# Performance work log

Measured on AMD Instinct MI355X. Metric: run time of the kernel, lower is better.

Reference implementation:

```python
import jax, jax.numpy as jnp
import numpy as np

DIM = 512
HEADS = 8
DIM_HEAD = 64
INNER = HEADS * DIM_HEAD  # 512
LN_EPS = 1e-5


def setup_inputs() -> dict:
    key = jax.random.key(0)
    ks = jax.random.split(key, 6)
    b, n = 2, 2048
    x = jax.random.normal(ks[0], (b, n, DIM), dtype=jnp.float32)
    # to_qkv: Linear(dim, inner*3, bias=False); torch weight is [out,in], apply as x @ W.T
    w_qkv = jax.random.normal(ks[1], (3 * INNER, DIM), dtype=jnp.float32) * (DIM ** -0.5)
    reattn_w = jax.random.normal(ks[2], (HEADS, HEADS), dtype=jnp.float32)
    ln_g = jnp.ones((HEADS,), dtype=jnp.float32)
    ln_b = jnp.zeros((HEADS,), dtype=jnp.float32)
    w_out = jax.random.normal(ks[3], (DIM, INNER), dtype=jnp.float32) * (INNER ** -0.5)
    b_out = jnp.zeros((DIM,), dtype=jnp.float32)
    return {"x": x, "w_qkv": w_qkv, "reattn_w": reattn_w,
            "ln_g": ln_g, "ln_b": ln_b, "w_out": w_out, "b_out": b_out}


def reference(x, w_qkv, reattn_w, ln_g, ln_b, w_out, b_out):
    b, n, _ = x.shape
    scale = DIM_HEAD ** -0.5
    qkv = x @ w_qkv.T  # [b, n, 3*inner]
    q, k, v = jnp.split(qkv, 3, axis=-1)
    # b n (h d) -> b h n d
    split_heads = lambda t: t.reshape(b, n, HEADS, DIM_HEAD).transpose(0, 2, 1, 3)
    q, k, v = split_heads(q), split_heads(k), split_heads(v)
    dots = jnp.einsum('bhid,bhjd->bhij', q, k) * scale
    attn = jax.nn.softmax(dots, axis=-1)
    # re-attention: cross-head mixing then LayerNorm over head dim
    attn = jnp.einsum('bhij,hg->bgij', attn, reattn_w)
    a = attn.transpose(0, 2, 3, 1)  # b i j h
    mu = jnp.mean(a, axis=-1, keepdims=True)
    var = jnp.mean((a - mu) ** 2, axis=-1, keepdims=True)
    a = (a - mu) * jax.lax.rsqrt(var + LN_EPS) * ln_g + ln_b
    attn = a.transpose(0, 3, 1, 2)  # b h i j
    out = jnp.einsum('bhij,bhjd->bhid', attn, v)
    out = out.transpose(0, 2, 1, 3).reshape(b, n, INNER)
    out = out @ w_out.T + b_out  # dropout p=0 -> identity
    return out
```

## Files before the change

### kernel.cpp

```cpp
#include <hip/hip_runtime.h>
#include <hip/hip_bf16.h>


typedef __attribute__((ext_vector_type(8))) short bfx8;
typedef __attribute__((ext_vector_type(4))) float f32x4;
typedef unsigned short u16;
typedef unsigned int u32;

#define QSCALE 0.18033688011112042f

static __device__ inline u16 f2bf(float f) {
  union { float f; unsigned u; } cv; cv.f = f;
  unsigned u = cv.u;
  u += 0x7fffu + ((u >> 16) & 1u);
  return (u16)(u >> 16);
}
static __device__ inline u32 cvtpk(float lo, float hi) {
  u32 d; asm("v_cvt_pk_bf16_f32 %0, %1, %2" : "=v"(d) : "v"(lo), "v"(hi)); return d;
}
static __device__ inline float fexp2(float x) {
  float r; asm("v_exp_f32 %0, %1" : "=v"(r) : "v"(x)); return r;
}
static __device__ inline float flog2(float x) {
  float r; asm("v_log_f32 %0, %1" : "=v"(r) : "v"(x)); return r;
}

__global__ __launch_bounds__(256) void convert3(
    const float* __restrict__ x, const float* __restrict__ wq,
    const float* __restrict__ wo,
    u16* __restrict__ xb, u16* __restrict__ wqb, u16* __restrict__ wob) {
  int e = (blockIdx.x * 256 + threadIdx.x) * 4;
  const float* src; u16* dst; int off;
  if (e < 2097152)      { src = x;  dst = xb;  off = e; }
  else if (e < 2883584) { src = wq; dst = wqb; off = e - 2097152; }
  else                  { src = wo; dst = wob; off = e - 2883584; }
  float4 v = *(const float4*)&src[off];
  ushort4 o; o.x = f2bf(v.x); o.y = f2bf(v.y); o.z = f2bf(v.z); o.w = f2bf(v.w);
  *(ushort4*)&dst[off] = o;
}

__global__ __launch_bounds__(256) void gemm_qkv(
    const u16* __restrict__ A, const u16* __restrict__ B,
    u16* __restrict__ qb, u16* __restrict__ kb, u16* __restrict__ vtb) {
  __shared__ u16 As[128 * 32];
  __shared__ u16 Bs[128 * 32];
  const int t = threadIdx.x, lane = t & 63;
  const int wm = (t >> 6) >> 1, wn = (t >> 6) & 1;
  const int m0 = blockIdx.y * 128, n0 = blockIdx.x * 128;
  const int li = lane & 15, lg = lane >> 4;
  const int rowA = t >> 2, kb8 = (t & 3) * 8;
  f32x4 acc[4][4] = {};
  for (int k0 = 0; k0 < 512; k0 += 32) {
    __syncthreads();
    *(bfx8*)&As[rowA * 32 + kb8]        = *(const bfx8*)&A[(size_t)(m0 + rowA) * 512 + k0 + kb8];
    *(bfx8*)&As[(rowA + 64) * 32 + kb8] = *(const bfx8*)&A[(size_t)(m0 + rowA + 64) * 512 + k0 + kb8];
    *(bfx8*)&Bs[rowA * 32 + kb8]        = *(const bfx8*)&B[(size_t)(n0 + rowA) * 512 + k0 + kb8];
    *(bfx8*)&Bs[(rowA + 64) * 32 + kb8] = *(const bfx8*)&B[(size_t)(n0 + rowA + 64) * 512 + k0 + kb8];
    __syncthreads();
    bfx8 af[4], bf_[4];
#pragma unroll
    for (int mi = 0; mi < 4; mi++)
      af[mi] = *(const bfx8*)&As[(wm * 64 + mi * 16 + li) * 32 + lg * 8];
#pragma unroll
    for (int ni = 0; ni < 4; ni++)
      bf_[ni] = *(const bfx8*)&Bs[(wn * 64 + ni * 16 + li) * 32 + lg * 8];
#pragma unroll
    for (int mi = 0; mi < 4; mi++)
#pragma unroll
      for (int ni = 0; ni < 4; ni++)
        acc[mi][ni] = __builtin_amdgcn_mfma_f32_16x16x32_bf16(af[mi], bf_[ni], acc[mi][ni], 0, 0, 0);
  }
#pragma unroll
  for (int mi = 0; mi < 4; mi++) {
#pragma unroll
    for (int ni = 0; ni < 4; ni++) {
      const int nc  = n0 + wn * 64 + ni * 16 + li;
      const int mrb = m0 + wm * 64 + mi * 16 + lg * 4;
      const int part = nc >> 9, within = nc & 511;
      const int h = within >> 6, d = within & 63;
      const int bb = mrb >> 11, ii = mrb & 2047;
      if (part == 0) {
#pragma unroll
        for (int r = 0; r < 4; r++)
          qb[(((size_t)bb * 8 + h) * 2048 + ii + r) * 64 + d] = f2bf(acc[mi][ni][r] * QSCALE);
      } else if (part == 1) {
#pragma unroll
        for (int r = 0; r < 4; r++)
          kb[(((size_t)bb * 8 + h) * 2048 + ii + r) * 64 + d] = f2bf(acc[mi][ni][r]);
      } else {
        ushort4 u;
        u.x = f2bf(acc[mi][ni][0]); u.y = f2bf(acc[mi][ni][1]);
        u.z = f2bf(acc[mi][ni][2]); u.w = f2bf(acc[mi][ni][3]);
        *(ushort4*)&vtb[(((size_t)bb * 8 + h) * 64 + d) * 2048 + ii] = u;
      }
    }
  }
}

__global__ __launch_bounds__(256) void passA(
    const u16* __restrict__ qb, const u16* __restrict__ kb,
    float2* __restrict__ statp) {
  const int t = threadIdx.x, lane = t & 63, w = t >> 6;
  const int bh = blockIdx.y, js = blockIdx.z;
  const int i0 = blockIdx.x * 64 + w * 16;
  const int li = lane & 15, lg = lane >> 4;
  const u16* Qh = qb + ((size_t)bh * 2048 + i0 + li) * 64;
  const u16* Kb = kb + (size_t)bh * 2048 * 64;
  const bfx8 q0 = *(const bfx8*)&Qh[lg * 8];
  const bfx8 q1 = *(const bfx8*)&Qh[32 + lg * 8];
  float m = -1e30f, l = 0.f;
  const int jbeg = js * 512, jend = jbeg + 512;
  for (int j0 = jbeg; j0 < jend; j0 += 32) {
    const u16* KhA = Kb + (size_t)(j0 + li) * 64;
    const u16* KhB = KhA + 16 * 64;
    bfx8 a0 = *(const bfx8*)&KhA[lg * 8];
    bfx8 a1 = *(const bfx8*)&KhA[32 + lg * 8];
    bfx8 b0 = *(const bfx8*)&KhB[lg * 8];
    bfx8 b1 = *(const bfx8*)&KhB[32 + lg * 8];
    __builtin_amdgcn_sched_barrier(0);
    f32x4 sa = {0.f, 0.f, 0.f, 0.f}, sb = {0.f, 0.f, 0.f, 0.f};
    sa = __builtin_amdgcn_mfma_f32_16x16x32_bf16(a0, q0, sa, 0, 0, 0);
    sa = __builtin_amdgcn_mfma_f32_16x16x32_bf16(a1, q1, sa, 0, 0, 0);
    sb = __builtin_amdgcn_mfma_f32_16x16x32_bf16(b0, q0, sb, 0, 0, 0);
    sb = __builtin_amdgcn_mfma_f32_16x16x32_bf16(b1, q1, sb, 0, 0, 0);
    float mt = fmaxf(fmaxf(fmaxf(sa[0], sa[1]), fmaxf(sa[2], sa[3])),
                     fmaxf(fmaxf(sb[0], sb[1]), fmaxf(sb[2], sb[3])));
    float mn = fmaxf(m, mt);
    float es = (fexp2(sa[0] - mn) + fexp2(sa[1] - mn)) + (fexp2(sa[2] - mn) + fexp2(sa[3] - mn))
             + (fexp2(sb[0] - mn) + fexp2(sb[1] - mn)) + (fexp2(sb[2] - mn) + fexp2(sb[3] - mn));
    l = fmaf(l, fexp2(m - mn), es);
    m = mn;
  }
  for (int off = 16; off < 64; off <<= 1) {
    float mo = __shfl_xor(m, off, 64);
    float lo = __shfl_xor(l, off, 64);
    float mn = fmaxf(m, mo);
    l = l * fexp2(m - mn) + lo * fexp2(mo - mn);
    m = mn;
  }
  if (lane < 16) statp[(size_t)js * 32768 + (size_t)bh * 2048 + i0 + li] = make_float2(m, l);
}

__global__ __launch_bounds__(512) __attribute__((amdgpu_waves_per_eu(4, 4)))
void passB(
    const u16* __restrict__ qb, const u16* __restrict__ kb,
    const u16* __restrict__ vtb, const float2* __restrict__ statp,
    const float* __restrict__ Wmix, const float* __restrict__ lng,
    const float* __restrict__ lnb, u16* __restrict__ innerP) {
  __shared__ __align__(16) u16 A2[8 * 16 * 128];
  __shared__ __align__(16) u16 Qs[8 * 16 * 72];
  const int t = threadIdx.x, lane = t & 63, w = t >> 6;
  const int b = blockIdx.y, i0 = blockIdx.x * 16;
  const int li = lane & 15, lg = lane >> 4;
  const int swz = (li & 7) << 3;

#pragma unroll
  for (int cc = 0; cc < 2; cc++) {
    const int c = t + cc * 512;
    const int h = c >> 7, qi = (c >> 3) & 15, d8 = c & 7;
    bfx8 v = *(const bfx8*)&qb[(((size_t)(b * 8 + h)) * 2048 + i0 + qi) * 64 + d8 * 8];
    *(bfx8*)&Qs[(h * 16 + qi) * 72 + d8 * 8] = v;
  }

  float wm_[8][8], lng_[8], lnb_[8];
#pragma unroll
  for (int h = 0; h < 8; h++)
#pragma unroll
    for (int g = 0; g < 8; g++) wm_[h][g] = Wmix[h * 8 + g];
#pragma unroll
  for (int g = 0; g < 8; g++) { lng_[g] = lng[g]; lnb_[g] = lnb[g]; }

  float stM[8];
#pragma unroll
  for (int h = 0; h < 8; h++) {
    const size_t idx = ((size_t)(b * 8 + h)) * 2048 + i0 + li;
    float m = -1e30f, l = 0.f;
#pragma unroll
    for (int z = 0; z < 4; z++) {
      const float2 a = statp[(size_t)z * 32768 + idx];
      const float mn = fmaxf(m, a.x);
      l = l * fexp2(m - mn) + a.y * fexp2(a.x - mn);
      m = mn;
    }
    stM[h] = m + flog2(l);
  }

  __syncthreads();

  f32x4 pacc[4] = {};
  const int jmb = blockIdx.z * 1024;
  const size_t hstr = (size_t)2048 * 64;
  for (int jm = jmb; jm < jmb + 1024; jm += 128) {
    const int j0 = jm + w * 16;
    const u16* Kb0 = kb + ((size_t)(b * 8) * 2048 + j0 + li) * 64;
    float p[8][4];
#pragma unroll
    for (int hb = 0; hb < 2; hb++) {
      bfx8 kf[4][2];
#pragma unroll
      for (int hh = 0; hh < 4; hh++) {
        const u16* Kh = Kb0 + (size_t)(hb * 4 + hh) * hstr;
        kf[hh][0] = *(const bfx8*)&Kh[lg * 8];
        kf[hh][1] = *(const bfx8*)&Kh[32 + lg * 8];
      }
      __builtin_amdgcn_sched_barrier(0);
#pragma unroll
      for (int hh = 0; hh < 4; hh++) {
        const int h = hb * 4 + hh;
        const bfx8 qA = *(const bfx8*)&Qs[(h * 16 + li) * 72 + lg * 8];
        const bfx8 qB = *(const bfx8*)&Qs[(h * 16 + li) * 72 + 32 + lg * 8];
        f32x4 s = {0.f, 0.f, 0.f, 0.f};
        s = __builtin_amdgcn_mfma_f32_16x16x32_bf16(kf[hh][0], qA, s, 0, 0, 0);
        s = __builtin_amdgcn_mfma_f32_16x16x32_bf16(kf[hh][1], qB, s, 0, 0, 0);
#pragma unroll
        for (int r = 0; r < 4; r++) p[h][r] = fexp2(s[r] - stM[h]);
      }
    }
    u32 apk[8][2];
#pragma unroll
    for (int r = 0; r < 4; r++) {
      float a_[8]; float sum = 0.f, sumsq = 0.f;
#pragma unroll
      for (int g = 0; g < 8; g++) {
        float acc = 0.f;
#pragma unroll
        for (int h = 0; h < 8; h++) acc = fmaf(p[h][r], wm_[h][g], acc);
        a_[g] = acc; sum += acc; sumsq = fmaf(acc, acc, sumsq);
      }
      const float mu = sum * 0.125f;
      const float var = fmaf(sumsq, 0.125f, -mu * mu);
      const float rs = rsqrtf(var + 1e-5f);
#pragma unroll
      for (int g = 0; g < 8; g++) {
        const float av = fmaf((a_[g] - mu) * rs, lng_[g], lnb_[g]);
        if (r & 1) apk[g][r >> 1] |= cvtpk(av, av) & 0xffff0000u;
        else       apk[g][r >> 1]  = cvtpk(av, av) & 0x0000ffffu;
      }
    }
    {
      const int jsw = (w * 16 + lg * 4) ^ swz;
#pragma unroll
      for (int g = 0; g < 8; g++)
        *(uint2*)&A2[(g * 16 + li) * 128 + jsw] = make_uint2(apk[g][0], apk[g][1]);
    }
    const u16* Vh = vtb + ((size_t)(b * 8 + w)) * 64 * 2048 + jm;
    bfx8 vF[4][4];
#pragma unroll
    for (int kc = 0; kc < 4; kc++)
#pragma unroll
      for (int nd = 0; nd < 4; nd++)
        vF[kc][nd] = *(const bfx8*)&Vh[(size_t)(nd * 16 + li) * 2048 + kc * 32 + lg * 8];
    __syncthreads();
    __builtin_amdgcn_s_setprio(1);
#pragma unroll
    for (int kc = 0; kc < 4; kc++) {
      const bfx8 af = *(const bfx8*)&A2[(w * 16 + li) * 128 + ((kc * 32 + lg * 8) ^ swz)];
#pragma unroll
      for (int nd = 0; nd < 4; nd++)
        pacc[nd] = __builtin_amdgcn_mfma_f32_16x16x32_bf16(af, vF[kc][nd], pacc[nd], 0, 0, 0);
    }
    __builtin_amdgcn_s_setprio(0);
    __syncthreads();
  }
  u16* dst = innerP + (size_t)blockIdx.z * 2097152 + ((size_t)b * 2048 + i0) * 512 + w * 64;
#pragma unroll
  for (int nd = 0; nd < 4; nd++)
#pragma unroll
    for (int r = 0; r < 4; r++)
      dst[(lg * 4 + r) * 512 + nd * 16 + li] = f2bf(pacc[nd][r]);
}

static __device__ inline bfx8 addbf8(bfx8 a, bfx8 b) {
  bfx8 r;
#pragma unroll
  for (int e = 0; e < 8; e += 2) {
    union { float f; u32 u; } a0, a1, b0, b1;
    a0.u = ((u32)(u16)a[e]) << 16;     b0.u = ((u32)(u16)b[e]) << 16;
    a1.u = ((u32)(u16)a[e + 1]) << 16; b1.u = ((u32)(u16)b[e + 1]) << 16;
    const u32 pk = cvtpk(a0.f + b0.f, a1.f + b1.f);
    r[e] = (short)(pk & 0xffff); r[e + 1] = (short)(pk >> 16);
  }
  return r;
}

__global__ __launch_bounds__(256) void gemm_out(
    const u16* __restrict__ A0, const u16* __restrict__ A1,
    const u16* __restrict__ B,
    float* __restrict__ outf, const float* __restrict__ bias) {
  __shared__ u16 As[128 * 32];
  __shared__ u16 Bs[128 * 32];
  const int t = threadIdx.x, lane = t & 63;
  const int wm = (t >> 6) >> 1, wn = (t >> 6) & 1;
  const int m0 = blockIdx.y * 128, n0 = blockIdx.x * 128;
  const int li = lane & 15, lg = lane >> 4;
  const int rowA = t >> 2, kb8 = (t & 3) * 8;
  f32x4 acc[4][4] = {};
  for (int k0 = 0; k0 < 512; k0 += 32) {
    __syncthreads();
    {
      const size_t iA = (size_t)(m0 + rowA) * 512 + k0 + kb8;
      const size_t iB = (size_t)(m0 + rowA + 64) * 512 + k0 + kb8;
      *(bfx8*)&As[rowA * 32 + kb8] =
          addbf8(*(const bfx8*)&A0[iA], *(const bfx8*)&A1[iA]);
      *(bfx8*)&As[(rowA + 64) * 32 + kb8] =
          addbf8(*(const bfx8*)&A0[iB], *(const bfx8*)&A1[iB]);
      *(bfx8*)&Bs[rowA * 32 + kb8]        = *(const bfx8*)&B[(size_t)(n0 + rowA) * 512 + k0 + kb8];
      *(bfx8*)&Bs[(rowA + 64) * 32 + kb8] = *(const bfx8*)&B[(size_t)(n0 + rowA + 64) * 512 + k0 + kb8];
    }
    __syncthreads();
    bfx8 af[4], bf_[4];
#pragma unroll
    for (int mi = 0; mi < 4; mi++)
      af[mi] = *(const bfx8*)&As[(wm * 64 + mi * 16 + li) * 32 + lg * 8];
#pragma unroll
    for (int ni = 0; ni < 4; ni++)
      bf_[ni] = *(const bfx8*)&Bs[(wn * 64 + ni * 16 + li) * 32 + lg * 8];
#pragma unroll
    for (int mi = 0; mi < 4; mi++)
#pragma unroll
      for (int ni = 0; ni < 4; ni++)
        acc[mi][ni] = __builtin_amdgcn_mfma_f32_16x16x32_bf16(af[mi], bf_[ni], acc[mi][ni], 0, 0, 0);
  }
#pragma unroll
  for (int mi = 0; mi < 4; mi++) {
#pragma unroll
    for (int ni = 0; ni < 4; ni++) {
      const int nc  = n0 + wn * 64 + ni * 16 + li;
      const int mrb = m0 + wm * 64 + mi * 16 + lg * 4;
      const float bv = bias[nc];
#pragma unroll
      for (int r = 0; r < 4; r++)
        outf[(size_t)(mrb + r) * 512 + nc] = acc[mi][ni][r] + bv;
    }
  }
}

extern "C" void kernel_launch(void* const* d_in, const int* in_sizes, int n_in,
                              void* d_out, int out_size, void* d_ws, size_t ws_size,
                              hipStream_t stream) {
  const float* x      = (const float*)d_in[0];
  const float* w_qkv  = (const float*)d_in[1];
  const float* reattn = (const float*)d_in[2];
  const float* ln_g   = (const float*)d_in[3];
  const float* ln_b   = (const float*)d_in[4];
  const float* w_out  = (const float*)d_in[5];
  const float* b_out  = (const float*)d_in[6];
  float* out = (float*)d_out;
  char* ws = (char*)d_ws;
  u16*    xb    = (u16*)(ws + 0);
  u16*    wqb   = (u16*)(ws + 4194304);
  u16*    innerP= (u16*)(ws + 0);
  u16*    qbf   = (u16*)(ws + 8388608);
  u16*    kbf   = (u16*)(ws + 12582912);
  u16*    vtb   = (u16*)(ws + 16777216);
  float2* statp = (float2*)(ws + 20971520);
  u16*    wob   = (u16*)(ws + 22020096);

  convert3<<<3072, 256, 0, stream>>>(x, w_qkv, w_out, xb, wqb, wob);
  gemm_qkv<<<dim3(12, 32), 256, 0, stream>>>(xb, wqb, qbf, kbf, vtb);
  passA<<<dim3(32, 16, 4), 256, 0, stream>>>(qbf, kbf, statp);
  passB<<<dim3(128, 2, 2), 512, 0, stream>>>(qbf, kbf, vtb, statp, reattn, ln_g, ln_b, innerP);
  gemm_out<<<dim3(4, 32), 256, 0, stream>>>(innerP, innerP + 2097152, wob, out, b_out);
}
```

Baseline: 227.9 us.

## Drop split-j partials in passB and hoist V loads ahead of scores

passB now walks the full key range in each block instead of splitting it across two z-slices. This removes the second partial output buffer and the bf16 add of the two partials inside gemm_out. The V fragment loads move to the top of each iteration so their latency overlaps the QK and re-attention math, and the bf16 packing now pairs two rows with one convert instead of masking. The occupancy hint is relaxed from exactly 4 to at least 2 waves per EU, which allows more registers. The cost is that only 256 blocks run instead of 512, each doing twice the work, so the GPU has less parallelism to fill it.

```diff
diff --git a/kernel.cpp b/kernel.cpp
--- a/kernel.cpp
+++ b/kernel.cpp
@@ -141,12 +141,12 @@
   if (lane < 16) statp[(size_t)js * 32768 + (size_t)bh * 2048 + i0 + li] = make_float2(m, l);
 }
 
-__global__ __launch_bounds__(512) __attribute__((amdgpu_waves_per_eu(4, 4)))
+__global__ __launch_bounds__(512) __attribute__((amdgpu_waves_per_eu(2)))
 void passB(
     const u16* __restrict__ qb, const u16* __restrict__ kb,
     const u16* __restrict__ vtb, const float2* __restrict__ statp,
     const float* __restrict__ Wmix, const float* __restrict__ lng,
-    const float* __restrict__ lnb, u16* __restrict__ innerP) {
+    const float* __restrict__ lnb, u16* __restrict__ inner) {
   __shared__ __align__(16) u16 A2[8 * 16 * 128];
   __shared__ __align__(16) u16 Qs[8 * 16 * 72];
   const int t = threadIdx.x, lane = t & 63, w = t >> 6;
@@ -188,9 +188,17 @@
   __syncthreads();
 
   f32x4 pacc[4] = {};
-  const int jmb = blockIdx.z * 1024;
   const size_t hstr = (size_t)2048 * 64;
-  for (int jm = jmb; jm < jmb + 1024; jm += 128) {
+  const u16* Vh = vtb + ((size_t)(b * 8 + w)) * 64 * 2048;
+  for (int jm = 0; jm < 2048; jm += 128) {
+    bfx8 vF[4][4];
+#pragma unroll
+    for (int kc = 0; kc < 4; kc++)
+#pragma unroll
+      for (int nd = 0; nd < 4; nd++)
+        vF[kc][nd] = *(const bfx8*)&Vh[(size_t)(nd * 16 + li) * 2048 + jm + kc * 32 + lg * 8];
+    __builtin_amdgcn_sched_barrier(0);
+
     const int j0 = jm + w * 16;
     const u16* Kb0 = kb + ((size_t)(b * 8) * 2048 + j0 + li) * 64;
     float p[8][4];
@@ -217,6 +225,7 @@
       }
     }
     u32 apk[8][2];
+    float tmp[8];
 #pragma unroll
     for (int r = 0; r < 4; r++) {
       float a_[8]; float sum = 0.f, sumsq = 0.f;
@@ -233,8 +242,8 @@
 #pragma unroll
       for (int g = 0; g < 8; g++) {
         const float av = fmaf((a_[g] - mu) * rs, lng_[g], lnb_[g]);
-        if (r & 1) apk[g][r >> 1] |= cvtpk(av, av) & 0xffff0000u;
-        else       apk[g][r >> 1]  = cvtpk(av, av) & 0x0000ffffu;
+        if (r & 1) apk[g][r >> 1] = cvtpk(tmp[g], av);
+        else       tmp[g] = av;
       }
     }
     {
@@ -243,13 +252,6 @@
       for (int g = 0; g < 8; g++)
         *(uint2*)&A2[(g * 16 + li) * 128 + jsw] = make_uint2(apk[g][0], apk[g][1]);
     }
-    const u16* Vh = vtb + ((size_t)(b * 8 + w)) * 64 * 2048 + jm;
-    bfx8 vF[4][4];
-#pragma unroll
-    for (int kc = 0; kc < 4; kc++)
-#pragma unroll
-      for (int nd = 0; nd < 4; nd++)
-        vF[kc][nd] = *(const bfx8*)&Vh[(size_t)(nd * 16 + li) * 2048 + kc * 32 + lg * 8];
     __syncthreads();
     __builtin_amdgcn_s_setprio(1);
 #pragma unroll
@@ -262,7 +264,7 @@
     __builtin_amdgcn_s_setprio(0);
     __syncthreads();
   }
-  u16* dst = innerP + (size_t)blockIdx.z * 2097152 + ((size_t)b * 2048 + i0) * 512 + w * 64;
+  u16* dst = inner + ((size_t)b * 2048 + i0) * 512 + w * 64;
 #pragma unroll
   for (int nd = 0; nd < 4; nd++)
 #pragma unroll
@@ -270,22 +272,8 @@
       dst[(lg * 4 + r) * 512 + nd * 16 + li] = f2bf(pacc[nd][r]);
 }
 
-static __device__ inline bfx8 addbf8(bfx8 a, bfx8 b) {
-  bfx8 r;
-#pragma unroll
-  for (int e = 0; e < 8; e += 2) {
-    union { float f; u32 u; } a0, a1, b0, b1;
-    a0.u = ((u32)(u16)a[e]) << 16;     b0.u = ((u32)(u16)b[e]) << 16;
-    a1.u = ((u32)(u16)a[e + 1]) << 16; b1.u = ((u32)(u16)b[e + 1]) << 16;
-    const u32 pk = cvtpk(a0.f + b0.f, a1.f + b1.f);
-    r[e] = (short)(pk & 0xffff); r[e + 1] = (short)(pk >> 16);
-  }
-  return r;
-}
-
 __global__ __launch_bounds__(256) void gemm_out(
-    const u16* __restrict__ A0, const u16* __restrict__ A1,
-    const u16* __restrict__ B,
+    const u16* __restrict__ A, const u16* __restrict__ B,
     float* __restrict__ outf, const float* __restrict__ bias) {
   __shared__ u16 As[128 * 32];
   __shared__ u16 Bs[128 * 32];
@@ -297,16 +285,10 @@
   f32x4 acc[4][4] = {};
   for (int k0 = 0; k0 < 512; k0 += 32) {
     __syncthreads();
-    {
-      const size_t iA = (size_t)(m0 + rowA) * 512 + k0 + kb8;
-      const size_t iB = (size_t)(m0 + rowA + 64) * 512 + k0 + kb8;
-      *(bfx8*)&As[rowA * 32 + kb8] =
-          addbf8(*(const bfx8*)&A0[iA], *(const bfx8*)&A1[iA]);
-      *(bfx8*)&As[(rowA + 64) * 32 + kb8] =
-          addbf8(*(const bfx8*)&A0[iB], *(const bfx8*)&A1[iB]);
-      *(bfx8*)&Bs[rowA * 32 + kb8]        = *(const bfx8*)&B[(size_t)(n0 + rowA) * 512 + k0 + kb8];
-      *(bfx8*)&Bs[(rowA + 64) * 32 + kb8] = *(const bfx8*)&B[(size_t)(n0 + rowA + 64) * 512 + k0 + kb8];
-    }
+    *(bfx8*)&As[rowA * 32 + kb8]        = *(const bfx8*)&A[(size_t)(m0 + rowA) * 512 + k0 + kb8];
+    *(bfx8*)&As[(rowA + 64) * 32 + kb8] = *(const bfx8*)&A[(size_t)(m0 + rowA + 64) * 512 + k0 + kb8];
+    *(bfx8*)&Bs[rowA * 32 + kb8]        = *(const bfx8*)&B[(size_t)(n0 + rowA) * 512 + k0 + kb8];
+    *(bfx8*)&Bs[(rowA + 64) * 32 + kb8] = *(const bfx8*)&B[(size_t)(n0 + rowA + 64) * 512 + k0 + kb8];
     __syncthreads();
     bfx8 af[4], bf_[4];
 #pragma unroll
@@ -349,7 +331,7 @@
   char* ws = (char*)d_ws;
   u16*    xb    = (u16*)(ws + 0);
   u16*    wqb   = (u16*)(ws + 4194304);
-  u16*    innerP= (u16*)(ws + 0);
+  u16*    inner = (u16*)(ws + 0);
   u16*    qbf   = (u16*)(ws + 8388608);
   u16*    kbf   = (u16*)(ws + 12582912);
   u16*    vtb   = (u16*)(ws + 16777216);
@@ -359,6 +341,6 @@
   convert3<<<3072, 256, 0, stream>>>(x, w_qkv, w_out, xb, wqb, wob);
   gemm_qkv<<<dim3(12, 32), 256, 0, stream>>>(xb, wqb, qbf, kbf, vtb);
   passA<<<dim3(32, 16, 4), 256, 0, stream>>>(qbf, kbf, statp);
-  passB<<<dim3(128, 2, 2), 512, 0, stream>>>(qbf, kbf, vtb, statp, reattn, ln_g, ln_b, innerP);
-  gemm_out<<<dim3(4, 32), 256, 0, stream>>>(innerP, innerP + 2097152, wob, out, b_out);
-}
+  passB<<<dim3(128, 2), 512, 0, stream>>>(qbf, kbf, vtb, statp, reattn, ln_g, ln_b, inner);
+  gemm_out<<<dim3(4, 32), 256, 0, stream>>>(inner, wob, out, b_out);
+}
```

After: 241.9 us. 6.1% more time.
